# Kernel tuning notes

Hardware: AMD Instinct MI355X
Metric: run time of the kernel (lower is better)

The kernel has to match this reference:

```python
import jax, jax.numpy as jnp
import numpy as np

B = 16384      # batch of Monte Carlo paths
N = 100        # time steps
DIM_W = 3
DT = 0.01
SQRT_DT = DT ** 0.5
SIGMA0 = 0.5   # constant diffusion coefficient (concrete sigma = SIGMA0 * ones(B,1,DIM_W))


def _mlp(x, W1, b1, W2, b2, W3, b3):
    h = jax.nn.relu(x @ W1 + b1)
    h = jax.nn.relu(h @ W2 + b2)
    return h @ W3 + b3


def setup_inputs() -> dict:
    key = jax.random.key(0)
    ks = jax.random.split(key, 8)
    s = 0.1  # modest weight scale for numerical sanity
    return {
        'y0': jnp.ones((1,), jnp.float32),
        'Y0': jnp.zeros((1, 1), jnp.float32),
        'zW1': s * jax.random.normal(ks[0], (2, 64), jnp.float32),
        'zb1': jnp.zeros((64,), jnp.float32),
        'zW2': s * jax.random.normal(ks[1], (64, 64), jnp.float32),
        'zb2': jnp.zeros((64,), jnp.float32),
        'zW3': s * jax.random.normal(ks[2], (64, 3), jnp.float32),
        'zb3': jnp.zeros((3,), jnp.float32),
        'qW1': s * jax.random.normal(ks[3], (2, 64), jnp.float32),
        'qb1': jnp.zeros((64,), jnp.float32),
        'qW2': s * jax.random.normal(ks[4], (64, 64), jnp.float32),
        'qb2': jnp.zeros((64,), jnp.float32),
        'qW3': s * jax.random.normal(ks[5], (64, 1), jnp.float32),
        'qb3': jnp.zeros((1,), jnp.float32),
        'dW': jax.random.normal(ks[6], (N, B, DIM_W), jnp.float32),
        'dZ': jax.random.normal(ks[7], (N, B, DIM_W), jnp.float32),
    }


def reference(y0, Y0, zW1, zb1, zW2, zb2, zW3, zb3,
              qW1, qb1, qW2, qb2, qW3, qb3, dW, dZ):
    y = jnp.broadcast_to(y0.reshape(1, 1), (B, 1))          # (B,1) state
    Y = jnp.broadcast_to(Y0, (B, 1))                         # (B,1) value process
    t = jnp.zeros((B, 1), jnp.float32)

    def step(carry, noise):
        y, Y, t, loss_acc = carry
        dWi, dZi = noise
        inp = jnp.concatenate([t, y], axis=1)                # (B,2)
        z = _mlp(inp, zW1, zb1, zW2, zb2, zW3, zb3)          # (B,3)
        q = _mlp(inp, qW1, qb1, qW2, qb2, qW3, qb3)          # (B,1)
        f = 0.5 * q * q                                      # generator (B,1)
        dw = dWi * SQRT_DT
        dz = dZi * SQRT_DT
        # sigma = SIGMA0 * ones(B,1,DIM_W); bmm(sigma, dw) = SIGMA0 * sum_j dw_j
        diffusion = SIGMA0 * jnp.sum(dw, axis=1, keepdims=True)
        y_new = y + q * DT + diffusion                       # mu = q
        Y_next = Y - f * DT + jnp.sum(z * dw, axis=1, keepdims=True)
        residual = Y_next - (Y - f * DT + jnp.sum(z * dz, axis=1, keepdims=True))
        loss_acc = loss_acc + jnp.mean(residual * residual)
        return (y_new, Y_next, t + DT, loss_acc), None

    (y, Y, t, total_residual_loss), _ = jax.lax.scan(
        step, (y, Y, t, jnp.float32(0.0)), (dW, dZ))
    terminal = y * y                                         # terminal_cost(y)
    terminal_loss = jnp.mean((Y - terminal) ** 2)
    return terminal_loss + total_residual_loss
```

## Files before the change

### kernel.cpp

```cpp
#include <hip/hip_runtime.h>
#include <hip/hip_bf16.h>

#define BATCH   16384
#define NSTEPS  100
#define DT_     0.01f
#define SQRTDT  0.1f
#define SIGMA0_ 0.5f

typedef _Float16  f16x2  __attribute__((ext_vector_type(2)));
typedef _Float16  f16x4  __attribute__((ext_vector_type(4)));
typedef _Float16  f16x8  __attribute__((ext_vector_type(8)));
typedef __fp16    h16x2  __attribute__((ext_vector_type(2)));
typedef float     f32x4  __attribute__((ext_vector_type(4)));

typedef const __attribute__((address_space(1))) void* gas_ptr;
typedef __attribute__((address_space(3))) void*       las_ptr;

__global__ void zero_out_kernel(float* out) { if (threadIdx.x == 0) out[0] = 0.0f; }

static __device__ __forceinline__ f16x4 pk4(const f32x4& d) {
    union { h16x2 h[2]; f16x4 v; } c;
    c.h[0] = __builtin_amdgcn_cvt_pkrtz(d[0], d[1]);
    c.h[1] = __builtin_amdgcn_cvt_pkrtz(d[2], d[3]);
    return c.v;
}

__launch_bounds__(256, 1)
__global__ void deepbsde_kernel(
    const float* __restrict__ y0,  const float* __restrict__ Y0,
    const float* __restrict__ zW1, const float* __restrict__ zb1,
    const float* __restrict__ zW2, const float* __restrict__ zb2,
    const float* __restrict__ zW3, const float* __restrict__ zb3,
    const float* __restrict__ qW1, const float* __restrict__ qb1,
    const float* __restrict__ qW2, const float* __restrict__ qb2,
    const float* __restrict__ qW3, const float* __restrict__ qb3,
    const float* __restrict__ dW,  const float* __restrict__ dZ,
    float* __restrict__ out)
{
    __shared__ __align__(16) char ring[4][8][384];

    const int tid  = threadIdx.x;
    const int lane = tid & 63;
    const int w    = tid >> 6;
    const int ln15 = lane & 15, q4 = lane >> 4;
    const int gw   = (blockIdx.x << 2) + w;
    const int pbase = gw << 4;

    f16x2 A1z[8], B1z[8], C1z[8], A1q[8], B1q[8], C1q[8];
#pragma unroll
    for (int m = 0; m < 8; ++m) {
        int i0 = 2*m, i1 = 2*m + 1;
        int k0 = 32*(i0 >> 3) + 8*q4 + (i0 & 7);
        int k1 = 32*(i1 >> 3) + 8*q4 + (i1 & 7);
        A1z[m] = (f16x2){(_Float16)zW1[k0],      (_Float16)zW1[k1]};
        B1z[m] = (f16x2){(_Float16)zW1[64 + k0], (_Float16)zW1[64 + k1]};
        C1z[m] = (f16x2){(_Float16)zb1[k0],      (_Float16)zb1[k1]};
        A1q[m] = (f16x2){(_Float16)qW1[k0],      (_Float16)qW1[k1]};
        B1q[m] = (f16x2){(_Float16)qW1[64 + k0], (_Float16)qW1[64 + k1]};
        C1q[m] = (f16x2){(_Float16)qb1[k0],      (_Float16)qb1[k1]};
    }

    f16x8 AfZ[4][2], AfQ[4][2];
#pragma unroll
    for (int tN = 0; tN < 4; ++tN)
#pragma unroll
        for (int f = 0; f < 2; ++f)
#pragma unroll
            for (int j = 0; j < 8; ++j) {
                int k = 32*f + 8*q4 + j, n = 16*tN + ln15;
                AfZ[tN][f][j] = (_Float16)zW2[k*64 + n];
                AfQ[tN][f][j] = (_Float16)qW2[k*64 + n];
            }

    f32x4 b2zv[4], b2qv[4];
#pragma unroll
    for (int tN = 0; tN < 4; ++tN)
#pragma unroll
        for (int r = 0; r < 4; ++r) {
            b2zv[tN][r] = zb2[16*tN + 4*q4 + r];
            b2qv[tN][r] = qb2[16*tN + 4*q4 + r];
        }

    const int c3 = ln15 & 3;
    f16x4 A3z[4], A3q[4];
#pragma unroll
    for (int tN = 0; tN < 4; ++tN)
#pragma unroll
        for (int j = 0; j < 4; ++j) {
            int n = 16*tN + 4*q4 + j;
            A3z[tN][j] = (_Float16)((c3 < 3)  ? zW3[n*3 + c3] : 0.0f);
            A3q[tN][j] = (_Float16)((c3 == 3) ? qW3[n]        : 0.0f);
        }

    float y = y0[0], Yv = Y0[0], t = 0.0f, acc = 0.0f;
    const float zb30 = zb3[0], zb31 = zb3[1], zb32 = zb3[2], qb30 = qb3[0];

    const f16x2 zero2h = {(_Float16)0.0f, (_Float16)0.0f};
    const f32x4 zero4  = {0.0f, 0.0f, 0.0f, 0.0f};

    auto fill = [&](int i) {
        if (lane < 24) {
            const char* g = (lane < 12)
                ? (const char*)dW + ((size_t)i * BATCH + pbase) * 12 + (size_t)lane * 16
                : (const char*)dZ + ((size_t)i * BATCH + pbase) * 12 + (size_t)(lane - 12) * 16;
            __builtin_amdgcn_global_load_lds((gas_ptr)g, (las_ptr)&ring[w][i & 7][0],
                                             16, 0, 0);
        }
    };
    fill(0); fill(1); fill(2); fill(3);

    auto body = [&](int i) {
        const float* sl = (const float*)&ring[w][i & 7][0];
        float nw0 = sl[ln15*3 + 0], nw1 = sl[ln15*3 + 1], nw2 = sl[ln15*3 + 2];
        float nz0 = sl[48 + ln15*3 + 0], nz1 = sl[48 + ln15*3 + 1], nz2 = sl[48 + ln15*3 + 2];

        _Float16 th = (_Float16)t, yh = (_Float16)y;
        const f16x2 tv = {th, th}, yv = {yh, yh};
        union { f16x2 h[4]; f16x8 v; } bz0, bz1, bq0, bq1;
#pragma unroll
        for (int m = 0; m < 8; ++m) {
            f16x2 hz = __builtin_elementwise_max((f16x2)(B1z[m]*yv + (A1z[m]*tv + C1z[m])), zero2h);
            f16x2 hq = __builtin_elementwise_max((f16x2)(B1q[m]*yv + (A1q[m]*tv + C1q[m])), zero2h);
            if (m < 4) { bz0.h[m] = hz;     bq0.h[m] = hq; }
            else       { bz1.h[m - 4] = hz; bq1.h[m - 4] = hq; }
        }

        f16x4 B3z[4], B3q[4];
#pragma unroll
        for (int tN = 0; tN < 4; ++tN) {
            f32x4 dz = b2zv[tN];
            dz = __builtin_amdgcn_mfma_f32_16x16x32_f16(AfZ[tN][0], bz0.v, dz, 0, 0, 0);
            dz = __builtin_amdgcn_mfma_f32_16x16x32_f16(AfZ[tN][1], bz1.v, dz, 0, 0, 0);
            f32x4 dq = b2qv[tN];
            dq = __builtin_amdgcn_mfma_f32_16x16x32_f16(AfQ[tN][0], bq0.v, dq, 0, 0, 0);
            dq = __builtin_amdgcn_mfma_f32_16x16x32_f16(AfQ[tN][1], bq1.v, dq, 0, 0, 0);
            B3z[tN] = pk4(__builtin_elementwise_max(dz, zero4));
            B3q[tN] = pk4(__builtin_elementwise_max(dq, zero4));
        }

        f32x4 P0 = zero4, P1 = zero4, P2 = zero4, P3 = zero4;
        P0 = __builtin_amdgcn_mfma_f32_16x16x16f16(A3z[0], B3z[0], P0, 0, 0, 0);
        P1 = __builtin_amdgcn_mfma_f32_16x16x16f16(A3z[1], B3z[1], P1, 0, 0, 0);
        P2 = __builtin_amdgcn_mfma_f32_16x16x16f16(A3z[2], B3z[2], P2, 0, 0, 0);
        P3 = __builtin_amdgcn_mfma_f32_16x16x16f16(A3z[3], B3z[3], P3, 0, 0, 0);
        P0 = __builtin_amdgcn_mfma_f32_16x16x16f16(A3q[0], B3q[0], P0, 0, 0, 0);
        P1 = __builtin_amdgcn_mfma_f32_16x16x16f16(A3q[1], B3q[1], P1, 0, 0, 0);
        P2 = __builtin_amdgcn_mfma_f32_16x16x16f16(A3q[2], B3q[2], P2, 0, 0, 0);
        P3 = __builtin_amdgcn_mfma_f32_16x16x16f16(A3q[3], B3q[3], P3, 0, 0, 0);
        f32x4 P = (P0 + P1) + (P2 + P3);

        float z0 = P[0] + zb30, z1 = P[1] + zb31, z2 = P[2] + zb32;
        float qv = P[3] + qb30;

        float dw0 = SQRTDT*nw0, dw1 = SQRTDT*nw1, dw2 = SQRTDT*nw2;
        float dz0 = SQRTDT*nz0, dz1 = SQRTDT*nz1, dz2 = SQRTDT*nz2;
        float zdw = fmaf(z2, dw2, fmaf(z1, dw1, z0*dw0));
        float zdz = fmaf(z2, dz2, fmaf(z1, dz1, z0*dz0));
        float f = 0.5f*qv*qv;
        Yv = Yv - f*DT_ + zdw;
        float r = zdw - zdz;
        acc = fmaf(r, r, acc);
        y = y + qv*DT_ + SIGMA0_*(dw0 + dw1 + dw2);
        t += DT_;
    };

#pragma unroll 1
    for (int i = 0; i < NSTEPS - 4; ++i) {
        __builtin_amdgcn_s_waitcnt(0x0F73);
        fill(i + 4);
        body(i);
    }
    __builtin_amdgcn_s_waitcnt(0x0F70);
#pragma unroll 1
    for (int i = NSTEPS - 4; i < NSTEPS; ++i) body(i);

    float dterm = Yv - y*y;
    acc = fmaf(dterm, dterm, acc);

    float val = (q4 == 0) ? acc : 0.0f;
#pragma unroll
    for (int off = 1; off < 64; off <<= 1) val += __shfl_xor(val, off);
    if (lane == 0) atomicAdd(out, val * (1.0f / BATCH));
}

extern "C" void kernel_launch(void* const* d_in, const int* in_sizes, int n_in,
                              void* d_out, int out_size, void* d_ws, size_t ws_size,
                              hipStream_t stream)
{
    zero_out_kernel<<<1, 64, 0, stream>>>((float*)d_out);
    deepbsde_kernel<<<256, 256, 0, stream>>>(
        (const float*)d_in[0],  (const float*)d_in[1],
        (const float*)d_in[2],  (const float*)d_in[3],
        (const float*)d_in[4],  (const float*)d_in[5],
        (const float*)d_in[6],  (const float*)d_in[7],
        (const float*)d_in[8],  (const float*)d_in[9],
        (const float*)d_in[10], (const float*)d_in[11],
        (const float*)d_in[12], (const float*)d_in[13],
        (const float*)d_in[14], (const float*)d_in[15],
        (float*)d_out);
}
```

Before: 178.3 us.

## Split z and q MLPs across separate waves with per-step LDS exchange

Each 16-path group is now handled by two waves: one computes the z network and one the q network. The q wave passes q to the z wave through shared memory every step, and a block barrier per step keeps them in lockstep. This halves the serial per-step dependency chain per wave and doubles the grid to 512 blocks with 2 blocks per CU, aiming to hide latency better. The cost is a block-wide barrier each step, extra LDS traffic, and duplicated y/t updates.

```diff
diff --git a/kernel.cpp b/kernel.cpp
--- a/kernel.cpp
+++ b/kernel.cpp
@@ -25,7 +25,7 @@
     return c.v;
 }
 
-__launch_bounds__(256, 1)
+__launch_bounds__(256, 2)
 __global__ void deepbsde_kernel(
     const float* __restrict__ y0,  const float* __restrict__ Y0,
     const float* __restrict__ zW1, const float* __restrict__ zb1,
@@ -37,30 +37,35 @@
     const float* __restrict__ dW,  const float* __restrict__ dZ,
     float* __restrict__ out)
 {
-    __shared__ __align__(16) char ring[4][8][384];
+    __shared__ __align__(16) char ring[2][8][384];
+    __shared__ float qx[2][2][16];
 
     const int tid  = threadIdx.x;
     const int lane = tid & 63;
     const int w    = tid >> 6;
+    const int g    = w & 1;
+    const bool isQ = (w >= 2);
     const int ln15 = lane & 15, q4 = lane >> 4;
-    const int gw   = (blockIdx.x << 2) + w;
+    const int gw   = (blockIdx.x << 1) + g;
     const int pbase = gw << 4;
 
-    f16x2 A1z[8], B1z[8], C1z[8], A1q[8], B1q[8], C1q[8];
+    const float* W1p = isQ ? qW1 : zW1;
+    const float* b1p = isQ ? qb1 : zb1;
+    const float* W2p = isQ ? qW2 : zW2;
+    const float* b2p = isQ ? qb2 : zb2;
+
+    f16x2 A1[8], B1[8], C1[8];
 #pragma unroll
     for (int m = 0; m < 8; ++m) {
         int i0 = 2*m, i1 = 2*m + 1;
         int k0 = 32*(i0 >> 3) + 8*q4 + (i0 & 7);
         int k1 = 32*(i1 >> 3) + 8*q4 + (i1 & 7);
-        A1z[m] = (f16x2){(_Float16)zW1[k0],      (_Float16)zW1[k1]};
-        B1z[m] = (f16x2){(_Float16)zW1[64 + k0], (_Float16)zW1[64 + k1]};
-        C1z[m] = (f16x2){(_Float16)zb1[k0],      (_Float16)zb1[k1]};
-        A1q[m] = (f16x2){(_Float16)qW1[k0],      (_Float16)qW1[k1]};
-        B1q[m] = (f16x2){(_Float16)qW1[64 + k0], (_Float16)qW1[64 + k1]};
-        C1q[m] = (f16x2){(_Float16)qb1[k0],      (_Float16)qb1[k1]};
-    }
-
-    f16x8 AfZ[4][2], AfQ[4][2];
+        A1[m] = (f16x2){(_Float16)W1p[k0],      (_Float16)W1p[k1]};
+        B1[m] = (f16x2){(_Float16)W1p[64 + k0], (_Float16)W1p[64 + k1]};
+        C1[m] = (f16x2){(_Float16)b1p[k0],      (_Float16)b1p[k1]};
+    }
+
+    f16x8 Af[4][2];
 #pragma unroll
     for (int tN = 0; tN < 4; ++tN)
 #pragma unroll
@@ -68,28 +73,26 @@
 #pragma unroll
             for (int j = 0; j < 8; ++j) {
                 int k = 32*f + 8*q4 + j, n = 16*tN + ln15;
-                AfZ[tN][f][j] = (_Float16)zW2[k*64 + n];
-                AfQ[tN][f][j] = (_Float16)qW2[k*64 + n];
+                Af[tN][f][j] = (_Float16)W2p[k*64 + n];
             }
 
-    f32x4 b2zv[4], b2qv[4];
+    f32x4 b2v[4];
 #pragma unroll
     for (int tN = 0; tN < 4; ++tN)
 #pragma unroll
-        for (int r = 0; r < 4; ++r) {
-            b2zv[tN][r] = zb2[16*tN + 4*q4 + r];
-            b2qv[tN][r] = qb2[16*tN + 4*q4 + r];
-        }
+        for (int r = 0; r < 4; ++r)
+            b2v[tN][r] = b2p[16*tN + 4*q4 + r];
 
     const int c3 = ln15 & 3;
-    f16x4 A3z[4], A3q[4];
+    f16x4 A3[4];
 #pragma unroll
     for (int tN = 0; tN < 4; ++tN)
 #pragma unroll
         for (int j = 0; j < 4; ++j) {
             int n = 16*tN + 4*q4 + j;
-            A3z[tN][j] = (_Float16)((c3 < 3)  ? zW3[n*3 + c3] : 0.0f);
-            A3q[tN][j] = (_Float16)((c3 == 3) ? qW3[n]        : 0.0f);
+            float wv = isQ ? ((c3 == 3) ? qW3[n]        : 0.0f)
+                           : ((c3 < 3)  ? zW3[n*3 + c3] : 0.0f);
+            A3[tN][j] = (_Float16)wv;
         }
 
     float y = y0[0], Yv = Y0[0], t = 0.0f, acc = 0.0f;
@@ -98,89 +101,130 @@
     const f16x2 zero2h = {(_Float16)0.0f, (_Float16)0.0f};
     const f32x4 zero4  = {0.0f, 0.0f, 0.0f, 0.0f};
 
-    auto fill = [&](int i) {
+    float z0 = 0.f, z1 = 0.f, z2 = 0.f;
+    float nw0 = 0.f, nw1 = 0.f, nw2 = 0.f, nz0 = 0.f, nz1 = 0.f, nz2 = 0.f;
+
+    auto fillz = [&](int i) {
         if (lane < 24) {
-            const char* g = (lane < 12)
+            const char* gp = (lane < 12)
                 ? (const char*)dW + ((size_t)i * BATCH + pbase) * 12 + (size_t)lane * 16
                 : (const char*)dZ + ((size_t)i * BATCH + pbase) * 12 + (size_t)(lane - 12) * 16;
-            __builtin_amdgcn_global_load_lds((gas_ptr)g, (las_ptr)&ring[w][i & 7][0],
+            __builtin_amdgcn_global_load_lds((gas_ptr)gp, (las_ptr)&ring[g][i & 7][0],
                                              16, 0, 0);
         }
     };
-    fill(0); fill(1); fill(2); fill(3);
-
-    auto body = [&](int i) {
-        const float* sl = (const float*)&ring[w][i & 7][0];
-        float nw0 = sl[ln15*3 + 0], nw1 = sl[ln15*3 + 1], nw2 = sl[ln15*3 + 2];
-        float nz0 = sl[48 + ln15*3 + 0], nz1 = sl[48 + ln15*3 + 1], nz2 = sl[48 + ln15*3 + 2];
+
+    auto compute = [&](int i) {
+        const float* sl = (const float*)&ring[g][i & 7][0];
+        if (isQ) {
+            const volatile float* sv = (const volatile float*)sl;
+            nw0 = sv[ln15*3 + 0]; nw1 = sv[ln15*3 + 1]; nw2 = sv[ln15*3 + 2];
+        } else {
+            nw0 = sl[ln15*3 + 0];      nw1 = sl[ln15*3 + 1];      nw2 = sl[ln15*3 + 2];
+            nz0 = sl[48 + ln15*3 + 0]; nz1 = sl[48 + ln15*3 + 1]; nz2 = sl[48 + ln15*3 + 2];
+        }
 
         _Float16 th = (_Float16)t, yh = (_Float16)y;
         const f16x2 tv = {th, th}, yv = {yh, yh};
-        union { f16x2 h[4]; f16x8 v; } bz0, bz1, bq0, bq1;
+        union { f16x2 h[4]; f16x8 v; } b0, b1;
 #pragma unroll
         for (int m = 0; m < 8; ++m) {
-            f16x2 hz = __builtin_elementwise_max((f16x2)(B1z[m]*yv + (A1z[m]*tv + C1z[m])), zero2h);
-            f16x2 hq = __builtin_elementwise_max((f16x2)(B1q[m]*yv + (A1q[m]*tv + C1q[m])), zero2h);
-            if (m < 4) { bz0.h[m] = hz;     bq0.h[m] = hq; }
-            else       { bz1.h[m - 4] = hz; bq1.h[m - 4] = hq; }
-        }
-
-        f16x4 B3z[4], B3q[4];
+            f16x2 h = __builtin_elementwise_max((f16x2)(B1[m]*yv + (A1[m]*tv + C1[m])), zero2h);
+            if (m < 4) b0.h[m] = h; else b1.h[m - 4] = h;
+        }
+
+        f16x4 B3[4];
 #pragma unroll
         for (int tN = 0; tN < 4; ++tN) {
-            f32x4 dz = b2zv[tN];
-            dz = __builtin_amdgcn_mfma_f32_16x16x32_f16(AfZ[tN][0], bz0.v, dz, 0, 0, 0);
-            dz = __builtin_amdgcn_mfma_f32_16x16x32_f16(AfZ[tN][1], bz1.v, dz, 0, 0, 0);
-            f32x4 dq = b2qv[tN];
-            dq = __builtin_amdgcn_mfma_f32_16x16x32_f16(AfQ[tN][0], bq0.v, dq, 0, 0, 0);
-            dq = __builtin_amdgcn_mfma_f32_16x16x32_f16(AfQ[tN][1], bq1.v, dq, 0, 0, 0);
-            B3z[tN] = pk4(__builtin_elementwise_max(dz, zero4));
-            B3q[tN] = pk4(__builtin_elementwise_max(dq, zero4));
+            f32x4 d = b2v[tN];
+            d = __builtin_amdgcn_mfma_f32_16x16x32_f16(Af[tN][0], b0.v, d, 0, 0, 0);
+            d = __builtin_amdgcn_mfma_f32_16x16x32_f16(Af[tN][1], b1.v, d, 0, 0, 0);
+            B3[tN] = pk4(__builtin_elementwise_max(d, zero4));
         }
 
         f32x4 P0 = zero4, P1 = zero4, P2 = zero4, P3 = zero4;
-        P0 = __builtin_amdgcn_mfma_f32_16x16x16f16(A3z[0], B3z[0], P0, 0, 0, 0);
-        P1 = __builtin_amdgcn_mfma_f32_16x16x16f16(A3z[1], B3z[1], P1, 0, 0, 0);
-        P2 = __builtin_amdgcn_mfma_f32_16x16x16f16(A3z[2], B3z[2], P2, 0, 0, 0);
-        P3 = __builtin_amdgcn_mfma_f32_16x16x16f16(A3z[3], B3z[3], P3, 0, 0, 0);
-        P0 = __builtin_amdgcn_mfma_f32_16x16x16f16(A3q[0], B3q[0], P0, 0, 0, 0);
-        P1 = __builtin_amdgcn_mfma_f32_16x16x16f16(A3q[1], B3q[1], P1, 0, 0, 0);
-        P2 = __builtin_amdgcn_mfma_f32_16x16x16f16(A3q[2], B3q[2], P2, 0, 0, 0);
-        P3 = __builtin_amdgcn_mfma_f32_16x16x16f16(A3q[3], B3q[3], P3, 0, 0, 0);
+        P0 = __builtin_amdgcn_mfma_f32_16x16x16f16(A3[0], B3[0], P0, 0, 0, 0);
+        P1 = __builtin_amdgcn_mfma_f32_16x16x16f16(A3[1], B3[1], P1, 0, 0, 0);
+        P2 = __builtin_amdgcn_mfma_f32_16x16x16f16(A3[2], B3[2], P2, 0, 0, 0);
+        P3 = __builtin_amdgcn_mfma_f32_16x16x16f16(A3[3], B3[3], P3, 0, 0, 0);
         f32x4 P = (P0 + P1) + (P2 + P3);
 
-        float z0 = P[0] + zb30, z1 = P[1] + zb31, z2 = P[2] + zb32;
-        float qv = P[3] + qb30;
-
-        float dw0 = SQRTDT*nw0, dw1 = SQRTDT*nw1, dw2 = SQRTDT*nw2;
-        float dz0 = SQRTDT*nz0, dz1 = SQRTDT*nz1, dz2 = SQRTDT*nz2;
-        float zdw = fmaf(z2, dw2, fmaf(z1, dw1, z0*dw0));
-        float zdz = fmaf(z2, dz2, fmaf(z1, dz1, z0*dz0));
-        float f = 0.5f*qv*qv;
-        Yv = Yv - f*DT_ + zdw;
-        float r = zdw - zdz;
-        acc = fmaf(r, r, acc);
-        y = y + qv*DT_ + SIGMA0_*(dw0 + dw1 + dw2);
-        t += DT_;
+        if (isQ) {
+            float qv = P[3] + qb30;
+            if (q4 == 0) *(volatile float*)&qx[i & 1][g][ln15] = qv;
+            float dw0 = SQRTDT*nw0, dw1 = SQRTDT*nw1, dw2 = SQRTDT*nw2;
+            y = y + qv*DT_ + SIGMA0_*(dw0 + dw1 + dw2);
+            t += DT_;
+        } else {
+            z0 = P[0] + zb30; z1 = P[1] + zb31; z2 = P[2] + zb32;
+        }
     };
+
+    auto post = [&](int i) {
+        if (!isQ) {
+            float qv = *(const volatile float*)&qx[i & 1][g][ln15];
+            float dw0 = SQRTDT*nw0, dw1 = SQRTDT*nw1, dw2 = SQRTDT*nw2;
+            float dz0 = SQRTDT*nz0, dz1 = SQRTDT*nz1, dz2 = SQRTDT*nz2;
+            float zdw = fmaf(z2, dw2, fmaf(z1, dw1, z0*dw0));
+            float zdz = fmaf(z2, dz2, fmaf(z1, dz1, z0*dz0));
+            float f = 0.5f*qv*qv;
+            Yv = Yv - f*DT_ + zdw;
+            float r = zdw - zdz;
+            acc = fmaf(r, r, acc);
+            y = y + qv*DT_ + SIGMA0_*(dw0 + dw1 + dw2);
+            t += DT_;
+        }
+    };
+
+    if (!isQ) {
+        fillz(0); fillz(1); fillz(2); fillz(3);
+        __builtin_amdgcn_s_waitcnt(0x0F73);
+    }
+    __builtin_amdgcn_s_barrier();
+    __builtin_amdgcn_sched_barrier(0);
 
 #pragma unroll 1
     for (int i = 0; i < NSTEPS - 4; ++i) {
-        __builtin_amdgcn_s_waitcnt(0x0F73);
-        fill(i + 4);
-        body(i);
-    }
-    __builtin_amdgcn_s_waitcnt(0x0F70);
-#pragma unroll 1
-    for (int i = NSTEPS - 4; i < NSTEPS; ++i) body(i);
-
-    float dterm = Yv - y*y;
-    acc = fmaf(dterm, dterm, acc);
-
-    float val = (q4 == 0) ? acc : 0.0f;
-#pragma unroll
-    for (int off = 1; off < 64; off <<= 1) val += __shfl_xor(val, off);
-    if (lane == 0) atomicAdd(out, val * (1.0f / BATCH));
+        if (!isQ) fillz(i + 4);
+        compute(i);
+        __builtin_amdgcn_s_waitcnt(0x0073);
+        __builtin_amdgcn_s_barrier();
+        __builtin_amdgcn_sched_barrier(0);
+        post(i);
+    }
+
+    compute(NSTEPS - 4);
+    __builtin_amdgcn_s_waitcnt(0x0072);
+    __builtin_amdgcn_s_barrier();
+    __builtin_amdgcn_sched_barrier(0);
+    post(NSTEPS - 4);
+
+    compute(NSTEPS - 3);
+    __builtin_amdgcn_s_waitcnt(0x0071);
+    __builtin_amdgcn_s_barrier();
+    __builtin_amdgcn_sched_barrier(0);
+    post(NSTEPS - 3);
+
+    compute(NSTEPS - 2);
+    __builtin_amdgcn_s_waitcnt(0x0070);
+    __builtin_amdgcn_s_barrier();
+    __builtin_amdgcn_sched_barrier(0);
+    post(NSTEPS - 2);
+
+    compute(NSTEPS - 1);
+    __builtin_amdgcn_s_waitcnt(0xC07F);
+    __builtin_amdgcn_s_barrier();
+    __builtin_amdgcn_sched_barrier(0);
+    post(NSTEPS - 1);
+
+    if (!isQ) {
+        float dterm = Yv - y*y;
+        acc = fmaf(dterm, dterm, acc);
+        float val = (q4 == 0) ? acc : 0.0f;
+#pragma unroll
+        for (int off = 1; off < 64; off <<= 1) val += __shfl_xor(val, off);
+        if (lane == 0) atomicAdd(out, val * (1.0f / BATCH));
+    }
 }
 
 extern "C" void kernel_launch(void* const* d_in, const int* in_sizes, int n_in,
@@ -188,7 +232,7 @@
                               hipStream_t stream)
 {
     zero_out_kernel<<<1, 64, 0, stream>>>((float*)d_out);
-    deepbsde_kernel<<<256, 256, 0, stream>>>(
+    deepbsde_kernel<<<512, 256, 0, stream>>>(
         (const float*)d_in[0],  (const float*)d_in[1],
         (const float*)d_in[2],  (const float*)d_in[3],
         (const float*)d_in[4],  (const float*)d_in[5],
```

Result: slower. 194.2 us (+8.9%).
